# Kernel optimization log

Measured on AMD Instinct MI355X. Metric: run time of the kernel, lower is better.

## Reference

```python
import jax, jax.numpy as jnp
import numpy as np

B, S, E, H = 4, 2048, 512, 8
D = E // H  # projection_dim per head


def setup_inputs() -> dict:
    key = jax.random.key(0)
    ks = jax.random.split(key, 5)
    scale = 1.0 / np.sqrt(E)
    return {
        "x": jax.random.normal(ks[0], (B, S, E), dtype=jnp.float32),
        "Wq": jax.random.normal(ks[1], (E, E), dtype=jnp.float32) * scale,
        "bq": jnp.zeros((E,), dtype=jnp.float32),
        "Wk": jax.random.normal(ks[2], (E, E), dtype=jnp.float32) * scale,
        "bk": jnp.zeros((E,), dtype=jnp.float32),
        "Wv": jax.random.normal(ks[3], (E, E), dtype=jnp.float32) * scale,
        "bv": jnp.zeros((E,), dtype=jnp.float32),
        "Wo": jax.random.normal(ks[4], (E, E), dtype=jnp.float32) * scale,
        "bo": jnp.zeros((E,), dtype=jnp.float32),
    }


def _split_heads(t):
    # [B,S,E] -> [B,H,S,D]
    b, s, _ = t.shape
    return t.reshape(b, s, H, D).transpose(0, 2, 1, 3)


def reference(x, Wq, bq, Wk, bk, Wv, bv, Wo, bo):
    q = _split_heads(x @ Wq + bq)  # [B,H,S,D]
    k = _split_heads(x @ Wk + bk)
    v = _split_heads(x @ Wv + bv)
    # materialized QK^T scores as in source: matmul -> scale -> softmax -> matmul
    score = jnp.einsum("bhqd,bhkd->bhqk", q, k) / jnp.sqrt(
        jnp.asarray(D, dtype=q.dtype)
    )
    weights = jax.nn.softmax(score, axis=-1)
    attn = jnp.einsum("bhqk,bhkd->bhqd", weights, v)  # [B,H,S,D]
    merged = attn.transpose(0, 2, 1, 3).reshape(x.shape[0], x.shape[1], E)
    return merged @ Wo + bo
```

## Files before the change

kernel.cpp:

```cpp
#include <hip/hip_runtime.h>
#include <hip/hip_bf16.h>
#include <stdint.h>

typedef __bf16 bf16;
typedef __bf16 bf16x2 __attribute__((ext_vector_type(2)));
typedef __bf16 bf16x4 __attribute__((ext_vector_type(4)));
typedef __bf16 bf16x8 __attribute__((ext_vector_type(8)));
typedef float f32x4 __attribute__((ext_vector_type(4)));
typedef float f32x16 __attribute__((ext_vector_type(16)));
typedef unsigned int u32x4 __attribute__((ext_vector_type(4)));
typedef int i32x2 __attribute__((ext_vector_type(2)));

#define AS1 __attribute__((address_space(1)))
#define AS3 __attribute__((address_space(3)))


__global__ void prep_kernel(const float* __restrict__ x,
                            const float* __restrict__ W0, const float* __restrict__ W1,
                            const float* __restrict__ W2, const float* __restrict__ W3,
                            bf16* __restrict__ xb, bf16* __restrict__ Wt) {
  __shared__ bf16 t[64][65];
  const int z = blockIdx.z;
  if (z < 4) {
    const float* W = z == 0 ? W0 : z == 1 ? W1 : z == 2 ? W2 : W3;
    bf16* dst = Wt + (size_t)z * 262144;
    const int c = threadIdx.x & 63, r0 = threadIdx.x >> 6;
    const int bn = blockIdx.x * 64, bk = blockIdx.y * 64;
#pragma unroll
    for (int i = 0; i < 16; ++i) {
      int r = r0 * 16 + i;
      t[c][r] = (bf16)W[(size_t)(bk + r) * 512 + bn + c];
    }
    __syncthreads();
#pragma unroll
    for (int i = 0; i < 16; ++i) {
      int n = r0 * 16 + i;
      dst[(size_t)(bn + n) * 512 + bk + c] = t[n][c];
    }
  } else {
    int bi = (z - 4) * 64 + blockIdx.y * 8 + blockIdx.x;
    int i = bi * 256 + threadIdx.x;
    float4 v = reinterpret_cast<const float4*>(x)[i];
    bf16x4 o = { (bf16)v.x, (bf16)v.y, (bf16)v.z, (bf16)v.w };
    *reinterpret_cast<bf16x4*>(xb + (size_t)i * 4) = o;
  }
}

template<int BN, int MODE>
__global__ __launch_bounds__(256, 4) void gemm64_kernel(
    const bf16* __restrict__ A, const bf16* __restrict__ Bt,
    const float* __restrict__ bq, const float* __restrict__ bk,
    const float* __restrict__ bv, bf16* __restrict__ out_bf,
    float* __restrict__ out_f, float qscale)
{
  constexpr int NT = BN / 32;
  __shared__ bf16 As[64 * 64];
  __shared__ bf16 Bs[BN * 64];
  const int tid = threadIdx.x, lane = tid & 63, w = tid >> 6;
  const int wm = w >> 1, wn = w & 1;
  const int m0 = blockIdx.x * 64, n0g = blockIdx.y * BN;
  const int cl = lane & 15, hi = lane >> 4;
  const int lr = lane >> 3;
  const int cofs = ((lane & 7) << 4) ^ (lr << 4);

  f32x4 acc[2][NT] = {};

  for (int kt = 0; kt < 512; kt += 64) {
    __syncthreads();
#pragma unroll
    for (int c = 0; c < 2; ++c) {
      int rA = m0 + w * 16 + c * 8 + lr;
      const void* srcA = (const char*)A + ((size_t)rA * 512 + kt) * 2 + cofs;
      void* dstA = (char*)As + w * 2048 + c * 1024;
      __builtin_amdgcn_global_load_lds((const AS1 void*)srcA, (AS3 void*)dstA, 16, 0, 0);
    }
#pragma unroll
    for (int c = 0; c < NT; ++c) {
      int rB = n0g + w * (BN / 4) + c * 8 + lr;
      const void* srcB = (const char*)Bt + ((size_t)rB * 512 + kt) * 2 + cofs;
      void* dstB = (char*)Bs + w * (BN / 4) * 128 + c * 1024;
      __builtin_amdgcn_global_load_lds((const AS1 void*)srcB, (AS3 void*)dstB, 16, 0, 0);
    }
    __syncthreads();
#pragma unroll
    for (int ks = 0; ks < 2; ++ks) {
      bf16x8 af[2], bfv[NT];
#pragma unroll
      for (int mt = 0; mt < 2; ++mt) {
        int r = wm * 32 + mt * 16 + cl;
        int cb = (ks * 64 + (hi << 4)) ^ ((r & 7) << 4);
        af[mt] = *(const bf16x8*)((const char*)As + r * 128 + cb);
      }
#pragma unroll
      for (int nt = 0; nt < NT; ++nt) {
        int r = wn * (BN / 2) + nt * 16 + cl;
        int cb = (ks * 64 + (hi << 4)) ^ ((r & 7) << 4);
        bfv[nt] = *(const bf16x8*)((const char*)Bs + r * 128 + cb);
      }
#pragma unroll
      for (int mt = 0; mt < 2; ++mt)
#pragma unroll
        for (int nt = 0; nt < NT; ++nt)
          acc[mt][nt] = __builtin_amdgcn_mfma_f32_16x16x32_bf16(af[mt], bfv[nt], acc[mt][nt], 0, 0, 0);
    }
  }

  if (MODE == 0) {
    const int which = n0g >> 9;
    const float* bias = which == 0 ? bq : (which == 1 ? bk : bv);
    const float scale = which == 0 ? qscale : 1.0f;
    bf16* outb = out_bf + (size_t)which * 4194304;
    const int ncol0 = n0g & 511;
#pragma unroll
    for (int mt = 0; mt < 2; ++mt) {
#pragma unroll
      for (int nt = 0; nt < NT; ++nt) {
        int row0 = m0 + wm * 32 + mt * 16 + hi * 4;
        int col = ncol0 + wn * (BN / 2) + nt * 16 + cl;
        float bvl = bias[col];
        int h = col >> 6, d = col & 63;
#pragma unroll
        for (int i = 0; i < 4; ++i) {
          float vv = (acc[mt][nt][i] + bvl) * scale;
          int row = row0 + i;
          int b = row >> 11, s = row & 2047;
          outb[(((size_t)(b * 8 + h)) * 2048 + s) * 64 + d] = (bf16)vv;
        }
      }
    }
  } else {
#pragma unroll
    for (int mt = 0; mt < 2; ++mt) {
#pragma unroll
      for (int nt = 0; nt < NT; ++nt) {
        int row0 = m0 + wm * 32 + mt * 16 + hi * 4;
        int col = n0g + wn * (BN / 2) + nt * 16 + cl;
        float bvl = bq[col];
#pragma unroll
        for (int i = 0; i < 4; ++i)
          out_f[(size_t)(row0 + i) * 512 + col] = acc[mt][nt][i] + bvl;
      }
    }
  }
}

__device__ __forceinline__ float xhalf_get(float x, int H) {
#if __has_builtin(__builtin_amdgcn_permlane32_swap)
  int xi = __builtin_bit_cast(int, x);
  i32x2 r = __builtin_amdgcn_permlane32_swap(xi, xi, false, false);
  return __builtin_bit_cast(float, H ? r[0] : r[1]);
#else
  (void)H;
  return __shfl_xor(x, 32);
#endif
}

__global__ __launch_bounds__(512, 4) void attn_kernel(
    const bf16* __restrict__ q, const bf16* __restrict__ k,
    const bf16* __restrict__ v, bf16* __restrict__ merged)
{
  __shared__ union SU {
    struct { bf16 K[2][2][4096]; bf16 V[2][2][4096]; } s;
    struct {
      float EPf[4][64][33];
      float Msh[8][32];
      float Lsh[8][32];
      bf16  EP[4][2304];
    } e;
  } u;
  __shared__ bf16 VT[2][4096];

  const int tid = threadIdx.x, lane = tid & 63, w = tid >> 6;
  const int wl = w & 3, half = w >> 2;
  const int ht = tid & 255;
  const int l31 = lane & 31, H = lane >> 5;
  const int bh = blockIdx.x, qb = blockIdx.y;
  const int b = bh >> 3, h = bh & 7;
  const int kv0 = half << 10;

  const bf16* Q  = q + (size_t)bh * 2048 * 64;
  const bf16* Kp = k + (size_t)bh * 2048 * 64;
  const bf16* Vp = v + (size_t)bh * 2048 * 64;

  const int q0 = qb * 128 + wl * 32;
  const int kp = ht & 31;
  const int dblk = (ht >> 5) * 8;

  const int lr8 = lane >> 3;
  const int lc = lane & 7;

#define STAGE_KV(BUF, KEYBASE)                                                            \
  {                                                                                       \
    _Pragma("unroll")                                                                     \
    for (int i = 0; i < 2; ++i) {                                                         \
      int row = wl * 16 + i * 8 + lr8;                                                    \
      const void* sK = (const char*)Kp + ((size_t)((KEYBASE) + row)) * 128 + ((lc ^ lr8) << 4); \
      void* dK = (char*)u.s.K[half][BUF] + wl * 2048 + i * 1024;                          \
      __builtin_amdgcn_global_load_lds((const AS1 void*)sK, (AS3 void*)dK, 16, 0, 0);     \
      const void* sV = (const char*)Vp + ((size_t)((KEYBASE) + row)) * 128 + ((lc ^ ((row >> 1) & 7)) << 4); \
      void* dV = (char*)u.s.V[half][BUF] + wl * 2048 + i * 1024;                          \
      __builtin_amdgcn_global_load_lds((const AS1 void*)sV, (AS3 void*)dV, 16, 0, 0);     \
    }                                                                                     \
  }

  bf16x8 qf[4];
#pragma unroll
  for (int s = 0; s < 4; ++s)
    qf[s] = *(const bf16x8*)(Q + (size_t)(q0 + l31) * 64 + s * 16 + H * 8);

  f32x16 oacc[2] = {};
  float m_run = -1e30f, l_run = 0.f;

  STAGE_KV(0, kv0);
  __syncthreads();

  int cur = 0;
  for (int kt0 = kv0; kt0 < kv0 + 1024; kt0 += 64) {
    {
      const char* vb = (const char*)u.s.V[half][cur];
      const int vofs = (((ht >> 5) ^ (kp & 7)) << 4);
      bf16x8 vs0 = *(const bf16x8*)(vb + (2 * kp) * 128 + vofs);
      bf16x8 vs1 = *(const bf16x8*)(vb + (2 * kp + 1) * 128 + vofs);
#pragma unroll
      for (int j = 0; j < 8; ++j) {
        int d = dblk + j;
        bf16x2 t = { vs0[j], vs1[j] };
        *(bf16x2*)((char*)&VT[half][0] + d * 128 + ((4 * kp) ^ ((d & 7) << 4))) = t;
      }
    }
    __syncthreads();

    if (kt0 + 64 < kv0 + 1024) STAGE_KV(cur ^ 1, kt0 + 64);

    const char* kb = (const char*)u.s.K[half][cur];

#pragma unroll
    for (int ct = 0; ct < 2; ++ct) {
      f32x16 sc = {};
      {
        const int krow = ct * 32 + l31;
        bf16x8 kf[4];
#pragma unroll
        for (int s = 0; s < 4; ++s)
          kf[s] = *(const bf16x8*)(kb + krow * 128 + ((s * 32 + H * 16) ^ ((l31 & 7) << 4)));
#pragma unroll
        for (int s = 0; s < 4; ++s)
          sc = __builtin_amdgcn_mfma_f32_32x32x16_bf16(kf[s], qf[s], sc, 0, 0, 0);
      }

      float mx[8];
#pragma unroll
      for (int r = 0; r < 8; ++r) mx[r] = fmaxf(sc[r], sc[r + 8]);
      float t0 = fmaxf(fmaxf(mx[0], mx[1]), mx[2]);
      float t1 = fmaxf(fmaxf(mx[3], mx[4]), mx[5]);
      float t2 = fmaxf(mx[6], mx[7]);
      float pmax = fmaxf(fmaxf(t0, t1), t2);
      pmax = fmaxf(pmax, xhalf_get(pmax, H));
      if (__any(pmax > m_run + 8.f)) {
        float mn = fmaxf(m_run, pmax);
        float alpha = exp2f(m_run - mn);
        m_run = mn;
        l_run *= alpha;
#pragma unroll
        for (int dt = 0; dt < 2; ++dt)
#pragma unroll
          for (int r = 0; r < 16; ++r) oacc[dt][r] *= alpha;
      }
#pragma unroll
      for (int r = 0; r < 16; ++r) sc[r] = exp2f(sc[r] - m_run);

      float sm[8];
#pragma unroll
      for (int r = 0; r < 8; ++r) sm[r] = sc[r] + sc[r + 8];
      l_run += ((sm[0] + sm[1]) + (sm[2] + sm[3])) + ((sm[4] + sm[5]) + (sm[6] + sm[7]));

#pragma unroll
      for (int hf = 0; hf < 2; ++hf) {
        const int ks = ct * 2 + hf;
        const int g0 = 8 * hf;
        bf16x2 pa0 = { (bf16)sc[g0 + 0], (bf16)sc[g0 + 1] };
        bf16x2 pa1 = { (bf16)sc[g0 + 2], (bf16)sc[g0 + 3] };
        bf16x2 pb0 = { (bf16)sc[g0 + 4], (bf16)sc[g0 + 5] };
        bf16x2 pb1 = { (bf16)sc[g0 + 6], (bf16)sc[g0 + 7] };
        unsigned a0 = __builtin_bit_cast(unsigned, pa0);
        unsigned a1 = __builtin_bit_cast(unsigned, pa1);
        unsigned b0 = __builtin_bit_cast(unsigned, pb0);
        unsigned b1 = __builtin_bit_cast(unsigned, pb1);
        u32x4 pw;
#if __has_builtin(__builtin_amdgcn_permlane32_swap)
        i32x2 r0 = __builtin_amdgcn_permlane32_swap((int)a0, (int)b0, false, false);
        i32x2 r1 = __builtin_amdgcn_permlane32_swap((int)a1, (int)b1, false, false);
        pw[0] = (unsigned)r0[0]; pw[1] = (unsigned)r1[0];
        pw[2] = (unsigned)r0[1]; pw[3] = (unsigned)r1[1];
#else
        unsigned oa0 = (unsigned)__shfl_xor((int)a0, 32);
        unsigned oa1 = (unsigned)__shfl_xor((int)a1, 32);
        unsigned ob0 = (unsigned)__shfl_xor((int)b0, 32);
        unsigned ob1 = (unsigned)__shfl_xor((int)b1, 32);
        pw[0] = H ? ob0 : a0; pw[1] = H ? ob1 : a1;
        pw[2] = H ? b0 : oa0; pw[3] = H ? b1 : oa1;
#endif
        bf16x8 pf = __builtin_bit_cast(bf16x8, pw);
#pragma unroll
        for (int dt = 0; dt < 2; ++dt) {
          int d = dt * 32 + l31;
          bf16x8 vf = *(const bf16x8*)((const char*)&VT[half][0] + d * 128 + ((ks * 32 + H * 16) ^ ((d & 7) << 4)));
          oacc[dt] = __builtin_amdgcn_mfma_f32_32x32x16_bf16(vf, pf, oacc[dt], 0, 0, 0);
        }
      }
    }

    __syncthreads();
    cur ^= 1;
  }

  l_run += xhalf_get(l_run, H);

  if (H == 0) { u.e.Msh[w][l31] = m_run; u.e.Lsh[w][l31] = l_run; }
  __syncthreads();
  const int pw2 = w ^ 4;
  float m_o = u.e.Msh[pw2][l31], l_o = u.e.Lsh[pw2][l31];
  float Mt = fmaxf(m_run, m_o);
  float denom = exp2f(m_run - Mt) * l_run + exp2f(m_o - Mt) * l_o;
  float scale = exp2f(m_run - Mt) / denom;
  if (w < 4) {
    float* ep = &u.e.EPf[wl][lane][0];
#pragma unroll
    for (int dt = 0; dt < 2; ++dt)
#pragma unroll
      for (int r = 0; r < 16; ++r) ep[dt * 16 + r] = oacc[dt][r] * scale;
  }
  __syncthreads();
  if (w >= 4) {
    const float* ep = &u.e.EPf[wl][lane][0];
#pragma unroll
    for (int dt = 0; dt < 2; ++dt)
#pragma unroll
      for (int r = 0; r < 16; ++r) {
        float val = ep[dt * 16 + r] + oacc[dt][r] * scale;
        int d = dt * 32 + (r & 3) + 8 * (r >> 2) + 4 * H;
        u.e.EP[wl][l31 * 72 + d] = (bf16)val;
      }
    __builtin_amdgcn_s_waitcnt(0);
#pragma unroll
    for (int g = 0; g < 4; ++g) {
      int qr = g * 8 + (lane >> 3);
      bf16x8 row = *(const bf16x8*)&u.e.EP[wl][qr * 72 + (lane & 7) * 8];
      *(bf16x8*)(merged + (size_t)(b * 2048 + q0 + qr) * 512 + h * 64 + (lane & 7) * 8) = row;
    }
  }
#undef STAGE_KV
}

extern "C" void kernel_launch(void* const* d_in, const int* in_sizes, int n_in,
                              void* d_out, int out_size, void* d_ws, size_t ws_size,
                              hipStream_t stream) {
  const float* x  = (const float*)d_in[0];
  const float* Wq = (const float*)d_in[1];
  const float* bq = (const float*)d_in[2];
  const float* Wk = (const float*)d_in[3];
  const float* bk = (const float*)d_in[4];
  const float* Wv = (const float*)d_in[5];
  const float* bv = (const float*)d_in[6];
  const float* Wo = (const float*)d_in[7];
  const float* bo = (const float*)d_in[8];
  float* out = (float*)d_out;

  char* ws = (char*)d_ws;
  bf16* xb  = (bf16*)(ws);
  bf16* wt  = (bf16*)(ws + 8388608);
  bf16* qkv = (bf16*)(ws + 10485760);
  bf16* mg  = (bf16*)(ws + 35651584);

  prep_kernel<<<dim3(8, 8, 68), 256, 0, stream>>>(x, Wq, Wk, Wv, Wo, xb, wt);

  const float qscale = 0.125f * 1.44269504088896f;
  gemm64_kernel<128, 0><<<dim3(128, 12), 256, 0, stream>>>(
      xb, wt, bq, bk, bv, qkv, nullptr, qscale);

  bf16* qs = qkv;
  bf16* kk = qkv + 4194304;
  bf16* vv = qkv + 8388608;

  attn_kernel<<<dim3(32, 16), 512, 0, stream>>>(qs, kk, vv, mg);

  gemm64_kernel<64, 1><<<dim3(128, 8), 256, 0, stream>>>(
      mg, wt + 786432, bo, nullptr, nullptr, nullptr, out, 1.0f);
}
```

Before: 106.9 us.

## Emit V pre-transposed from projection GEMM and drop in-attention V transpose

The QKV projection epilogue now writes V in a [B,H,D,S] layout, transposing through a shared-memory tile with vectorized stores. The attention kernel then stages V^T straight into LDS with async global-to-LDS loads. This removes the per-tile LDS transpose of V and one barrier per KV iteration, and frees the separate VT shared buffer. The cost is an extra barrier pair and LDS round trip in the GEMM epilogue for the V blocks.

```diff
diff --git a/kernel.cpp b/kernel.cpp
--- a/kernel.cpp
+++ b/kernel.cpp
@@ -54,8 +54,10 @@
     float* __restrict__ out_f, float qscale)
 {
   constexpr int NT = BN / 32;
-  __shared__ bf16 As[64 * 64];
-  __shared__ bf16 Bs[BN * 64];
+  __shared__ union GU {
+    struct { bf16 As[64 * 64]; bf16 Bs[BN * 64]; } g;
+    bf16 tr[BN][72];
+  } su;
   const int tid = threadIdx.x, lane = tid & 63, w = tid >> 6;
   const int wm = w >> 1, wn = w & 1;
   const int m0 = blockIdx.x * 64, n0g = blockIdx.y * BN;
@@ -71,14 +73,14 @@
     for (int c = 0; c < 2; ++c) {
       int rA = m0 + w * 16 + c * 8 + lr;
       const void* srcA = (const char*)A + ((size_t)rA * 512 + kt) * 2 + cofs;
-      void* dstA = (char*)As + w * 2048 + c * 1024;
+      void* dstA = (char*)su.g.As + w * 2048 + c * 1024;
       __builtin_amdgcn_global_load_lds((const AS1 void*)srcA, (AS3 void*)dstA, 16, 0, 0);
     }
 #pragma unroll
     for (int c = 0; c < NT; ++c) {
       int rB = n0g + w * (BN / 4) + c * 8 + lr;
       const void* srcB = (const char*)Bt + ((size_t)rB * 512 + kt) * 2 + cofs;
-      void* dstB = (char*)Bs + w * (BN / 4) * 128 + c * 1024;
+      void* dstB = (char*)su.g.Bs + w * (BN / 4) * 128 + c * 1024;
       __builtin_amdgcn_global_load_lds((const AS1 void*)srcB, (AS3 void*)dstB, 16, 0, 0);
     }
     __syncthreads();
@@ -89,13 +91,13 @@
       for (int mt = 0; mt < 2; ++mt) {
         int r = wm * 32 + mt * 16 + cl;
         int cb = (ks * 64 + (hi << 4)) ^ ((r & 7) << 4);
-        af[mt] = *(const bf16x8*)((const char*)As + r * 128 + cb);
+        af[mt] = *(const bf16x8*)((const char*)su.g.As + r * 128 + cb);
       }
 #pragma unroll
       for (int nt = 0; nt < NT; ++nt) {
         int r = wn * (BN / 2) + nt * 16 + cl;
         int cb = (ks * 64 + (hi << 4)) ^ ((r & 7) << 4);
-        bfv[nt] = *(const bf16x8*)((const char*)Bs + r * 128 + cb);
+        bfv[nt] = *(const bf16x8*)((const char*)su.g.Bs + r * 128 + cb);
       }
 #pragma unroll
       for (int mt = 0; mt < 2; ++mt)
@@ -111,20 +113,48 @@
     const float scale = which == 0 ? qscale : 1.0f;
     bf16* outb = out_bf + (size_t)which * 4194304;
     const int ncol0 = n0g & 511;
-#pragma unroll
-    for (int mt = 0; mt < 2; ++mt) {
-#pragma unroll
-      for (int nt = 0; nt < NT; ++nt) {
-        int row0 = m0 + wm * 32 + mt * 16 + hi * 4;
-        int col = ncol0 + wn * (BN / 2) + nt * 16 + cl;
-        float bvl = bias[col];
+    if (which == 2) {
+      __syncthreads();
+#pragma unroll
+      for (int mt = 0; mt < 2; ++mt) {
+#pragma unroll
+        for (int nt = 0; nt < NT; ++nt) {
+          int dloc = wn * (BN / 2) + nt * 16 + cl;
+          float bvl = bias[ncol0 + dloc];
+#pragma unroll
+          for (int i = 0; i < 4; ++i) {
+            int s_loc = wm * 32 + mt * 16 + hi * 4 + i;
+            su.tr[dloc][s_loc] = (bf16)(acc[mt][nt][i] + bvl);
+          }
+        }
+      }
+      __syncthreads();
+      const int b = m0 >> 11, sbase = m0 & 2047;
+#pragma unroll
+      for (int pass = 0; pass < 4; ++pass) {
+        int dloc = pass * 32 + (tid >> 3);
+        int s0 = (tid & 7) * 8;
+        int col = ncol0 + dloc;
         int h = col >> 6, d = col & 63;
-#pragma unroll
-        for (int i = 0; i < 4; ++i) {
-          float vv = (acc[mt][nt][i] + bvl) * scale;
-          int row = row0 + i;
-          int b = row >> 11, s = row & 2047;
-          outb[(((size_t)(b * 8 + h)) * 2048 + s) * 64 + d] = (bf16)vv;
+        bf16x8 rowv = *(const bf16x8*)&su.tr[dloc][s0];
+        *(bf16x8*)(outb + ((size_t)((b * 8 + h) * 64 + d)) * 2048 + sbase + s0) = rowv;
+      }
+    } else {
+#pragma unroll
+      for (int mt = 0; mt < 2; ++mt) {
+#pragma unroll
+        for (int nt = 0; nt < NT; ++nt) {
+          int row0 = m0 + wm * 32 + mt * 16 + hi * 4;
+          int col = ncol0 + wn * (BN / 2) + nt * 16 + cl;
+          float bvl = bias[col];
+          int h = col >> 6, d = col & 63;
+#pragma unroll
+          for (int i = 0; i < 4; ++i) {
+            float vv = (acc[mt][nt][i] + bvl) * scale;
+            int row = row0 + i;
+            int b = row >> 11, s = row & 2047;
+            outb[(((size_t)(b * 8 + h)) * 2048 + s) * 64 + d] = (bf16)vv;
+          }
         }
       }
     }
@@ -157,10 +187,10 @@
 
 __global__ __launch_bounds__(512, 4) void attn_kernel(
     const bf16* __restrict__ q, const bf16* __restrict__ k,
-    const bf16* __restrict__ v, bf16* __restrict__ merged)
+    const bf16* __restrict__ vt, bf16* __restrict__ merged)
 {
   __shared__ union SU {
-    struct { bf16 K[2][2][4096]; bf16 V[2][2][4096]; } s;
+    struct { bf16 K[2][2][4096]; bf16 VT[2][2][4096]; } s;
     struct {
       float EPf[4][64][33];
       float Msh[8][32];
@@ -168,24 +198,19 @@
       bf16  EP[4][2304];
     } e;
   } u;
-  __shared__ bf16 VT[2][4096];
 
   const int tid = threadIdx.x, lane = tid & 63, w = tid >> 6;
   const int wl = w & 3, half = w >> 2;
-  const int ht = tid & 255;
   const int l31 = lane & 31, H = lane >> 5;
   const int bh = blockIdx.x, qb = blockIdx.y;
   const int b = bh >> 3, h = bh & 7;
   const int kv0 = half << 10;
 
-  const bf16* Q  = q + (size_t)bh * 2048 * 64;
-  const bf16* Kp = k + (size_t)bh * 2048 * 64;
-  const bf16* Vp = v + (size_t)bh * 2048 * 64;
+  const bf16* Q   = q  + (size_t)bh * 2048 * 64;
+  const bf16* Kp  = k  + (size_t)bh * 2048 * 64;
+  const bf16* Vtp = vt + (size_t)bh * 64 * 2048;
 
   const int q0 = qb * 128 + wl * 32;
-  const int kp = ht & 31;
-  const int dblk = (ht >> 5) * 8;
-
   const int lr8 = lane >> 3;
   const int lc = lane & 7;
 
@@ -197,8 +222,8 @@
       const void* sK = (const char*)Kp + ((size_t)((KEYBASE) + row)) * 128 + ((lc ^ lr8) << 4); \
       void* dK = (char*)u.s.K[half][BUF] + wl * 2048 + i * 1024;                          \
       __builtin_amdgcn_global_load_lds((const AS1 void*)sK, (AS3 void*)dK, 16, 0, 0);     \
-      const void* sV = (const char*)Vp + ((size_t)((KEYBASE) + row)) * 128 + ((lc ^ ((row >> 1) & 7)) << 4); \
-      void* dV = (char*)u.s.V[half][BUF] + wl * 2048 + i * 1024;                          \
+      const void* sV = (const char*)Vtp + (size_t)row * 4096 + (size_t)(KEYBASE) * 2 + ((lc ^ lr8) << 4); \
+      void* dV = (char*)u.s.VT[half][BUF] + wl * 2048 + i * 1024;                         \
       __builtin_amdgcn_global_load_lds((const AS1 void*)sV, (AS3 void*)dV, 16, 0, 0);     \
     }                                                                                     \
   }
@@ -216,23 +241,10 @@
 
   int cur = 0;
   for (int kt0 = kv0; kt0 < kv0 + 1024; kt0 += 64) {
-    {
-      const char* vb = (const char*)u.s.V[half][cur];
-      const int vofs = (((ht >> 5) ^ (kp & 7)) << 4);
-      bf16x8 vs0 = *(const bf16x8*)(vb + (2 * kp) * 128 + vofs);
-      bf16x8 vs1 = *(const bf16x8*)(vb + (2 * kp + 1) * 128 + vofs);
-#pragma unroll
-      for (int j = 0; j < 8; ++j) {
-        int d = dblk + j;
-        bf16x2 t = { vs0[j], vs1[j] };
-        *(bf16x2*)((char*)&VT[half][0] + d * 128 + ((4 * kp) ^ ((d & 7) << 4))) = t;
-      }
-    }
-    __syncthreads();
-
     if (kt0 + 64 < kv0 + 1024) STAGE_KV(cur ^ 1, kt0 + 64);
 
-    const char* kb = (const char*)u.s.K[half][cur];
+    const char* kb  = (const char*)u.s.K[half][cur];
+    const char* vtb = (const char*)u.s.VT[half][cur];
 
 #pragma unroll
     for (int ct = 0; ct < 2; ++ct) {
@@ -304,7 +316,7 @@
 #pragma unroll
         for (int dt = 0; dt < 2; ++dt) {
           int d = dt * 32 + l31;
-          bf16x8 vf = *(const bf16x8*)((const char*)&VT[half][0] + d * 128 + ((ks * 32 + H * 16) ^ ((d & 7) << 4)));
+          bf16x8 vf = *(const bf16x8*)(vtb + d * 128 + ((ks * 32 + H * 16) ^ ((d & 7) << 4)));
           oacc[dt] = __builtin_amdgcn_mfma_f32_32x32x16_bf16(vf, pf, oacc[dt], 0, 0, 0);
         }
       }
```

New measurement: 99.26 us (median of 2 runs). 1.08x faster.
